# Kernel tuning notes

Measured on AMD Instinct MI355X. Metric: run time of the kernel, lower is better.

## Reference

```python
import jax, jax.numpy as jnp
import numpy as np

B, NUM_CLASSES, G = 8, 80, 100
IMG = 1280
STRIDES = (8, 16, 32)
EPS = 1e-7            # mmyolo EPS in -log(iou + EPS)
IOU_EPS = 1e-6        # BboxOverlaps2D union eps
INF = 1e8
SOFT_CENTER_RADIUS = 3.0
TOPK = 13
IOU_WEIGHT = 3.0


def _make_priors():
    ps = []
    for s in STRIDES:
        n = IMG // s
        c = (jnp.arange(n, dtype=jnp.float32) + 0.5) * s
        yy, xx = jnp.meshgrid(c, c, indexing='ij')
        st = jnp.full((n * n,), float(s), jnp.float32)
        ps.append(jnp.stack([xx.ravel(), yy.ravel(), st, st], axis=-1))
    return jnp.concatenate(ps, axis=0)  # [N, 4] = (cx, cy, stride_x, stride_y)


def setup_inputs() -> dict:
    key = jax.random.key(0)
    k = jax.random.split(key, 8)
    priors = _make_priors()
    N = priors.shape[0]  # 33600
    # predicted boxes jittered around anchor points, xyxy
    cxcy = priors[None, :, :2] + jax.random.normal(k[0], (B, N, 2)) * priors[None, :, 2:3] * 2.0
    wh = priors[None, :, 2:3] * (1.0 + 4.0 * jax.random.uniform(k[1], (B, N, 2)))
    pred_bboxes = jnp.concatenate([cxcy - wh / 2, cxcy + wh / 2], axis=-1)
    pred_scores = jax.random.normal(k[2], (B, N, NUM_CLASSES)) * 2.0 - 2.0  # logits
    # gt boxes inside the image, xyxy
    x1y1 = jax.random.uniform(k[3], (B, G, 2)) * (IMG - 200)
    gwh = 20.0 + jax.random.uniform(k[4], (B, G, 2)) * 180.0
    gt_bboxes = jnp.concatenate([x1y1, x1y1 + gwh], axis=-1)
    gt_labels = jax.random.randint(k[5], (B, G, 1), 0, NUM_CLASSES)
    counts = jax.random.randint(k[6], (B,), 10, G + 1)
    pad_bbox_flag = (jnp.arange(G)[None, :] < counts[:, None]).astype(jnp.float32)[..., None]
    return {"pred_bboxes": pred_bboxes, "pred_scores": pred_scores, "priors": priors,
            "gt_labels": gt_labels, "gt_bboxes": gt_bboxes, "pad_bbox_flag": pad_bbox_flag}


def _pairwise_iou(b1, b2):
    # b1 [B,N,4], b2 [B,G,4] in xyxy -> [B,N,G]
    a1 = (b1[..., 2] - b1[..., 0]) * (b1[..., 3] - b1[..., 1])
    a2 = (b2[..., 2] - b2[..., 0]) * (b2[..., 3] - b2[..., 1])
    lt = jnp.maximum(b1[:, :, None, :2], b2[:, None, :, :2])
    rb = jnp.minimum(b1[:, :, None, 2:], b2[:, None, :, 2:])
    wh = jnp.clip(rb - lt, 0.0)
    overlap = wh[..., 0] * wh[..., 1]
    union = a1[:, :, None] + a2[:, None, :] - overlap
    return overlap / jnp.maximum(union, IOU_EPS)


def reference(pred_bboxes, pred_scores, priors, gt_labels, gt_bboxes, pad_bbox_flag):
    Bb, N, _ = pred_bboxes.shape
    Gg = gt_bboxes.shape[1]
    centers = priors[:, :2]
    valid_gt = pad_bbox_flag[..., 0] > 0  # [B,G]

    # point-in-box test (strict >0, as in find_inside_points)
    lt = centers[None, :, None, :] - gt_bboxes[:, None, :, :2]   # [B,N,G,2]
    rb = gt_bboxes[:, None, :, 2:] - centers[None, :, None, :]
    is_in = (jnp.minimum(jnp.min(lt, -1), jnp.min(rb, -1)) > 0) & valid_gt[:, None, :]
    valid_mask = jnp.any(is_in, -1)  # [B,N]

    # soft center prior
    gt_center = (gt_bboxes[..., :2] + gt_bboxes[..., 2:]) / 2.0
    strides = priors[:, 2]
    dist = jnp.sqrt(jnp.sum((centers[None, :, None, :] - gt_center[:, None, :, :]) ** 2, -1))
    dist = dist / strides[None, :, None] * valid_mask[..., None].astype(dist.dtype)
    soft_center_prior = jnp.power(10.0, dist - SOFT_CENTER_RADIUS)

    # IoU cost
    ious = _pairwise_iou(pred_bboxes, gt_bboxes)  # [B,N,G]
    iou_cost = -jnp.log(ious + EPS) * IOU_WEIGHT

    # classification cost: gather pred score of each gt's class
    lbl = jnp.broadcast_to(gt_labels[:, None, :, 0], (Bb, N, Gg))
    x = jnp.take_along_axis(pred_scores, lbl, axis=2)  # logits [B,N,G]
    scale = ious - jax.nn.sigmoid(x)
    bce = jax.nn.softplus(x) - x * ious  # BCE-with-logits, target=ious
    cls_cost = bce * (scale * scale)

    cost = cls_cost + iou_cost + soft_center_prior
    cost = jnp.where(valid_mask[..., None], cost, INF)

    # dynamic k per gt = clamp(int(sum of top-13 ious), min 1)
    k = min(TOPK, N)
    topk_ious = jax.lax.top_k(jnp.swapaxes(ious, 1, 2), k)[0]  # [B,G,k]
    dyn_k = jnp.maximum(jnp.sum(topk_ious, -1).astype(jnp.int32), 1)  # [B,G]

    # rank of each prior's cost within its gt column (ascending)
    ranks = jnp.argsort(jnp.argsort(cost, axis=1), axis=1)
    matching = (ranks < dyn_k[:, None, :]) & valid_gt[:, None, :]  # [B,N,G]

    # resolve priors matched to multiple gts: keep min-cost gt
    multi = jnp.sum(matching, -1) > 1  # [B,N]
    argmin_g = jnp.argmin(cost, axis=-1)
    onehot = argmin_g[..., None] == jnp.arange(Gg)[None, None, :]
    matching = jnp.where(multi[..., None], onehot, matching)

    fg = jnp.any(matching, -1)                       # [B,N]
    matched_gt = jnp.argmax(matching, -1)            # [B,N]
    matched_ious = jnp.sum(jnp.where(matching, ious, 0.0), -1)

    lbls = jnp.take_along_axis(gt_labels[..., 0], matched_gt, axis=1)
    assigned_labels = jnp.where(fg, lbls, NUM_CLASSES)
    assigned_labels_weights = jnp.ones((Bb, N), pred_scores.dtype)
    boxes = jnp.take_along_axis(gt_bboxes, matched_gt[..., None], axis=1)
    assigned_bboxes = jnp.where(fg[..., None], boxes, 0.0)
    assign_metrics = jnp.where(fg, matched_ious, 0.0)
    return assigned_labels, assigned_labels_weights, assigned_bboxes, assign_metrics
```

## Files before the change

kernel.cpp:

```cpp
#include <hip/hip_runtime.h>
#include <stdint.h>

#define BDIM 256
#define B_   8
#define NCLS 80
#define G_   100
#define N_   33600
#define TOPK_ 13
#define NCHUNK 2
#define TILES 525
#define CAPC 160
#define CAPI 160
#define INFC 1e8f


__device__ __forceinline__ unsigned int fkey(float f){
  unsigned int u = __float_as_uint(f);
  return (u & 0x80000000u) ? ~u : (u | 0x80000000u);
}
__device__ __forceinline__ float unfkey(unsigned int k){
  unsigned int u = (k & 0x80000000u) ? (k & 0x7fffffffu) : ~k;
  return __uint_as_float(u);
}

__device__ __forceinline__ float cost_eval(float iou, float x, float dist, bool valid){
  #pragma clang fp contract(off)
  float prior = exp2f((dist - 3.0f) * 3.321928094887362f);
  float iouc  = -logf(iou + 1e-7f) * 3.0f;
  float sig   = 1.0f / (1.0f + expf(-x));
  float sc    = iou - sig;
  float bce   = fmaxf(x, 0.0f) + log1pf(expf(-fabsf(x))) - x * iou;
  float c     = bce * (sc * sc) + iouc + prior;
  return valid ? c : INFC;
}

__device__ __forceinline__ unsigned long long wave_min_u64(unsigned long long v){
  #pragma unroll
  for (int m = 1; m < 64; m <<= 1){
    unsigned int lo = (unsigned int)__shfl_xor((int)(unsigned int)v, m, 64);
    unsigned int hi = (unsigned int)__shfl_xor((int)(unsigned int)(v >> 32), m, 64);
    unsigned long long o = ((unsigned long long)hi << 32) | lo;
    v = o < v ? o : v;
  }
  return v;
}

__device__ __forceinline__ void tile_params(int t, int& W, int& base, int& trow, int& tcol,
                                            float& s, float& invs){
  if (t < 400){            W = 160; base = 0;     s = 8.0f;  invs = 0.125f;
    trow = (t/20)*8;  tcol = (t - (t/20)*20)*8; }
  else if (t < 500){ int u = t - 400; W = 80; base = 25600; s = 16.0f; invs = 0.0625f;
    trow = (u/10)*8; tcol = (u - (u/10)*10)*8; }
  else {             int u = t - 500; W = 40; base = 32000; s = 32.0f; invs = 0.03125f;
    trow = (u/5)*8;  tcol = (u - (u/5)*5)*8; }
}

__device__ unsigned long long compact_cost(unsigned long long* buf, int cnt){
  const int lane = threadIdx.x & 63;
  unsigned long long a0 = (lane       < cnt) ? buf[lane]       : ~0ull;
  unsigned long long a1 = (lane + 64  < cnt) ? buf[lane + 64]  : ~0ull;
  unsigned long long a2 = (lane + 128 < cnt) ? buf[lane + 128] : ~0ull;
  unsigned long long mykeep = ~0ull, t13 = ~0ull;
  #pragma unroll
  for (int r = 0; r < TOPK_; ++r){
    unsigned long long v = a0 < a1 ? a0 : a1; v = v < a2 ? v : a2;
    unsigned long long mn = wave_min_u64(v);
    if      (a0 == mn) a0 = ~0ull;
    else if (a1 == mn) a1 = ~0ull;
    else if (a2 == mn) a2 = ~0ull;
    if (lane == r) mykeep = mn;
    t13 = mn;
  }
  if (lane < TOPK_) buf[lane] = mykeep;
  return t13;
}

__device__ float compact_iou(float* buf, int cnt){
  const int lane = threadIdx.x & 63;
  float a0 = (lane       < cnt) ? buf[lane]       : -1.0f;
  float a1 = (lane + 64  < cnt) ? buf[lane + 64]  : -1.0f;
  float a2 = (lane + 128 < cnt) ? buf[lane + 128] : -1.0f;
  float mykeep = -1.0f, t13 = -1.0f;
  #pragma unroll
  for (int r = 0; r < TOPK_; ++r){
    float mx = fmaxf(fmaxf(a0, a1), a2);
    #pragma unroll
    for (int m = 1; m < 64; m <<= 1) mx = fmaxf(mx, __shfl_xor(mx, m, 64));
    bool h0 = (a0 == mx), h1 = (a1 == mx), h2 = (a2 == mx);
    unsigned long long ball = __ballot(h0 | h1 | h2);
    int src = (int)(__ffsll(ball) - 1);
    if (lane == src){
      if (h0) a0 = -1.0f; else if (h1) a1 = -1.0f; else a2 = -1.0f;
    }
    if (lane == r) mykeep = mx;
    t13 = mx;
  }
  if (lane < TOPK_) buf[lane] = mykeep;
  return t13;
}


__global__ void __launch_bounds__(BDIM) k_validmask(
    const float* __restrict__ priors,
    const float* __restrict__ gt_bboxes,
    const float* __restrict__ pad_flag,
    unsigned char* __restrict__ valid_mask,
    uint32_t* __restrict__ match_mask)
{
  int b = blockIdx.y;
  __shared__ float4 sbox[G_];
  __shared__ float  sflag[G_];
  for (int g = threadIdx.x; g < G_; g += BDIM){
    sbox[g]  = ((const float4*)gt_bboxes)[b*G_ + g];
    sflag[g] = pad_flag[b*G_ + g];
  }
  __syncthreads();
  int n = blockIdx.x*BDIM + threadIdx.x;
  if (n >= N_) return;
  float cx = priors[n*4+0], cy = priors[n*4+1];
  bool v = false;
  for (int g = 0; g < G_; ++g){
    float4 gb = sbox[g];
    bool in = (cx - gb.x > 0.0f) & (cy - gb.y > 0.0f) &
              (gb.z - cx > 0.0f) & (gb.w - cy > 0.0f) & (sflag[g] > 0.0f);
    v |= in;
  }
  size_t idx = (size_t)b*N_ + n;
  valid_mask[idx] = v ? 1 : 0;
  ((uint4*)match_mask)[idx] = make_uint4(0u,0u,0u,0u);
}


__global__ void __launch_bounds__(64) k_tileprep(
    const float* __restrict__ pred_bboxes,
    const unsigned char* __restrict__ valid_mask,
    float4* __restrict__ tile_agg,
    uint32_t* __restrict__ tile_flag)
{
  int t = blockIdx.x, b = blockIdx.y, l = threadIdx.x;
  int W, base, trow, tcol; float s, invs;
  tile_params(t, W, base, trow, tcol, s, invs);
  int n = base + (trow + (l >> 3))*W + tcol + (l & 7);
  size_t idx = (size_t)b*N_ + n;
  float4 pb = ((const float4*)pred_bboxes)[idx];
  int v = valid_mask[idx];
  float x1 = pb.x, y1 = pb.y, x2 = pb.z, y2 = pb.w;
  #pragma unroll
  for (int m = 1; m < 64; m <<= 1){
    x1 = fminf(x1, __shfl_xor(x1, m, 64));
    y1 = fminf(y1, __shfl_xor(y1, m, 64));
    x2 = fmaxf(x2, __shfl_xor(x2, m, 64));
    y2 = fmaxf(y2, __shfl_xor(y2, m, 64));
  }
  unsigned long long anyb = __ballot(v != 0);
  if (l == 0){
    tile_agg [(size_t)b*TILES + t] = make_float4(x1, y1, x2, y2);
    tile_flag[(size_t)b*TILES + t] = (anyb != 0ull) ? 1u : 0u;
  }
}


__global__ void __launch_bounds__(BDIM) k_topk(
    const float* __restrict__ pred_bboxes,
    const float* __restrict__ pred_scores,
    const int*   __restrict__ gt_labels,
    const float* __restrict__ gt_bboxes,
    const float* __restrict__ pad_flag,
    const unsigned char* __restrict__ valid_mask,
    const float4* __restrict__ tile_agg,
    const uint32_t* __restrict__ tile_flag,
    unsigned long long* __restrict__ ck_out,
    float* __restrict__ ci_out)
{
  #pragma clang fp contract(off)
  const int g = blockIdx.x, b = blockIdx.y, chunk = blockIdx.z;
  if (pad_flag[b*G_ + g] <= 0.0f) return;

  __shared__ unsigned long long s_cbuf[4][CAPC];
  __shared__ float s_ibuf[4][CAPI];
  __shared__ unsigned long long s_fk[4][TOPK_ + 1];
  __shared__ float s_fi[4][TOPK_ + 1];

  const int tid = threadIdx.x, lane = tid & 63, wid = tid >> 6;
  unsigned long long* cbuf = s_cbuf[wid];
  float* ibuf = s_ibuf[wid];

  const float4 gb = ((const float4*)gt_bboxes)[b*G_ + g];
  const float ga  = (gb.z - gb.x) * (gb.w - gb.y);
  const float gcx = (gb.x + gb.z) * 0.5f, gcy = (gb.y + gb.w) * 0.5f;
  const int lbl = gt_labels[b*G_ + g];
  const unsigned int KEYINF = fkey(INFC);

  const float4* pb4 = (const float4*)pred_bboxes + (size_t)b*N_;
  const unsigned char* vm = valid_mask + (size_t)b*N_;
  const float* sc_b = pred_scores + (size_t)b*N_*NCLS;
  const float4* tag = tile_agg + (size_t)b*TILES;
  const uint32_t* tfl = tile_flag + (size_t)b*TILES;

  auto seed_eval = [&](int t, float& cst, float& iouv){
    #pragma clang fp contract(off)
    int nk, bs; float s, invs;
    if      (t < 25){ nk = 160; bs = 0;     s = 8.0f;  invs = 0.125f;   }
    else if (t < 50){ nk = 80;  bs = 25600; s = 16.0f; invs = 0.0625f;  }
    else            { nk = 40;  bs = 32000; s = 32.0f; invs = 0.03125f; }
    int rem = (t < 25) ? t : ((t < 50) ? t - 25 : t - 50);
    int r = rem / 5, c = rem - 5*r;
    int ix = (int)(gcx / s) - 2, iy = (int)(gcy / s) - 2;
    ix = ix < 0 ? 0 : (ix > nk-5 ? nk-5 : ix);
    iy = iy < 0 ? 0 : (iy > nk-5 ? nk-5 : iy);
    int col = ix + c, row = iy + r;
    int n = bs + row*nk + col;
    float4 pb = pb4[n];
    float pa = (pb.z - pb.x) * (pb.w - pb.y);
    float lx = fmaxf(pb.x, gb.x), ly = fmaxf(pb.y, gb.y);
    float rx = fminf(pb.z, gb.z), ry = fminf(pb.w, gb.w);
    float ov = fmaxf(rx - lx, 0.0f) * fmaxf(ry - ly, 0.0f);
    float un = pa + ga - ov;
    float iou = ov / fmaxf(un, 1e-6f);
    iouv = iou;
    bool valid = vm[n] != 0;
    float px = ((float)col + 0.5f)*s, py = ((float)row + 0.5f)*s;
    float dx = px - gcx, dy = py - gcy;
    float dist = sqrtf(dx*dx + dy*dy) * invs;
    float x = valid ? sc_b[(size_t)n*NCLS + lbl] : 0.0f;
    cst = cost_eval(iou, x, dist, valid);
  };

  float c0 = 3e38f, c1 = 3e38f, i0 = -1.0f, i1 = -1.0f;
  seed_eval(lane, c0, i0);
  if (lane < 11) seed_eval(lane + 64, c1, i1);

  float T = INFC;
  {
    const float lvs[7] = {47.0f, 24.0f, 12.0f, 6.0f, 3.0f, 1.5f, 0.75f};
    #pragma unroll
    for (int i = 0; i < 7; ++i){
      int cnt = __popcll(__ballot(c0 <= lvs[i])) + __popcll(__ballot(c1 <= lvs[i]));
      if (cnt >= TOPK_) T = lvs[i];
    }
  }
  float Tiou_m = 0.0f;
  {
    const float ivs[8] = {0.02f, 0.05f, 0.1f, 0.15f, 0.22f, 0.3f, 0.4f, 0.5f};
    #pragma unroll
    for (int i = 0; i < 8; ++i){
      int cnt = __popcll(__ballot(i0 >= ivs[i])) + __popcll(__ballot(i1 >= ivs[i]));
      if (cnt >= TOPK_) Tiou_m = ivs[i] * 0.999f;
    }
  }
  unsigned long long Tkey = ((unsigned long long)fkey(T) << 32) | 0xFFFFFFFFull;
  bool  tc48  = T < 48.0f;
  float gt_   = 3.02f + log10f(T);
  float gthr2 = gt_ * gt_;

  int ccnt = 0, icnt = 0;

  int sweep_nend = 0;
  if (chunk == 0 && wid == 0 && T == INFC){
    int found = 0, base = 0;
    while (found < TOPK_ && base < N_){
      int n = base + lane;
      bool inv = (vm[n] == 0);
      unsigned long long m = __ballot(inv);
      int pc = __popcll(m);
      int pos = ccnt + (int)__popcll(m & ((1ull << lane) - 1ull));
      if (inv) cbuf[pos] = ((unsigned long long)KEYINF << 32) | (unsigned)n;
      ccnt += pc;
      found += pc;
      base += 64;
    }
    sweep_nend = base;
  }

  const int lo_c = (chunk == 0) ? 0 : 263;
  const int hi_c = (chunk == 0) ? 263 : TILES;
  const int per  = (hi_c - lo_c + 3) >> 2;
  const int lo_w = lo_c + wid*per;
  const int hi_w = min(hi_c, lo_w + per);

  for (int tb = lo_w; tb < hi_w; tb += 64){
    int tt2 = tb + lane;
    bool pass = false;
    if (tt2 < hi_w){
      float4 ag = tag[tt2];
      uint32_t fl2 = tfl[tt2];
      int W, bse, trow, tcol; float s, invs;
      tile_params(tt2, W, bse, trow, tcol, s, invs);
      bool inter = (fminf(ag.z, gb.z) > fmaxf(ag.x, gb.x)) &&
                   (fminf(ag.w, gb.w) > fmaxf(ag.y, gb.y));
      float rx0 = ((float)tcol + 0.5f)*s, rx1 = ((float)tcol + 7.5f)*s;
      float ry0 = ((float)trow + 0.5f)*s, ry1 = ((float)trow + 7.5f)*s;
      float ddx = fmaxf(0.0f, fmaxf(rx0 - gcx, gcx - rx1));
      float ddy = fmaxf(0.0f, fmaxf(ry0 - gcy, gcy - ry1));
      float md2s = (ddx*ddx + ddy*ddy) * (invs*invs);
      bool costok = (fl2 != 0) && (md2s <= gthr2) && (inter || !tc48);
      pass = inter || costok;
    }
    unsigned long long pm = __ballot(pass);
    while (pm){
      int bit = (int)(__ffsll(pm) - 1);
      pm &= pm - 1ull;
      const int tt = tb + bit;

      int W, bse, trow, tcol; float s, invs;
      tile_params(tt, W, bse, trow, tcol, s, invs);
      int row = trow + (lane >> 3), col = tcol + (lane & 7);
      int n = bse + row*W + col;
      float px = ((float)col + 0.5f)*s, py = ((float)row + 0.5f)*s;
      float4 pb = pb4[n];
      float pa = (pb.z - pb.x) * (pb.w - pb.y);
      float lx = fmaxf(pb.x, gb.x), ly = fmaxf(pb.y, gb.y);
      float rx = fminf(pb.z, gb.z), ry = fminf(pb.w, gb.w);
      float ov = fmaxf(rx - lx, 0.0f) * fmaxf(ry - ly, 0.0f);
      float un = pa + ga - ov;
      bool ipass = ov > Tiou_m * un;

      float dx = px - gcx, dy = py - gcy;
      float dist2 = dx*dx + dy*dy;
      float d2s = dist2 * (invs * invs);
      bool valid = vm[n] != 0;
      bool needcost = valid && (d2s <= gthr2) && !((ov <= 0.0f) && tc48);

      float iou = 0.0f;
      if (__any(ipass || needcost)){
        if (ipass || needcost) iou = ov / fmaxf(un, 1e-6f);
      }

      {
        unsigned long long m = __ballot(ipass);
        if (m){
          int pc = __popcll(m);
          if (icnt + pc > CAPI){
            float t = compact_iou(ibuf, icnt); icnt = TOPK_;
            Tiou_m = t * 0.999f;
          }
          int pos = icnt + (int)__popcll(m & ((1ull << lane) - 1ull));
          if (ipass) ibuf[pos] = iou;
          icnt += pc;
        }
      }

      unsigned long long key = ((unsigned long long)KEYINF << 32) | (unsigned)n;
      bool cpass = (!valid) && (key < Tkey) && (n >= sweep_nend);
      if (__any(needcost)){
        if (needcost){
          float x = sc_b[(size_t)n*NCLS + lbl];
          float dist = sqrtf(dist2) * invs;
          float c = cost_eval(iou, x, dist, true);
          key = ((unsigned long long)fkey(c) << 32) | (unsigned)n;
          cpass = key < Tkey;
        }
      }
      {
        unsigned long long m = __ballot(cpass);
        if (m){
          int pc = __popcll(m);
          if (ccnt + pc > CAPC){
            Tkey = compact_cost(cbuf, ccnt); ccnt = TOPK_;
            float Tc = unfkey((unsigned int)(Tkey >> 32));
            tc48 = Tc < 48.0f;
            float gq = 3.02f + log10f(Tc);
            gthr2 = (gq > 0.0f) ? gq*gq : 1e30f;
          }
          int pos = ccnt + (int)__popcll(m & ((1ull << lane) - 1ull));
          if (cpass) cbuf[pos] = key;
          ccnt += pc;
        }
      }
    }
  }

  compact_cost(cbuf, ccnt);
  compact_iou(ibuf, icnt);
  if (lane < TOPK_){ s_fk[wid][lane] = cbuf[lane]; s_fi[wid][lane] = ibuf[lane]; }
  if (lane == TOPK_){ s_fk[wid][TOPK_] = ~0ull; s_fi[wid][TOPK_] = -1e30f; }
  __syncthreads();

  if (tid == 0){
    size_t base = (((size_t)b*G_ + g)*NCHUNK + chunk)*TOPK_;
    {
      int p0 = 0, p1 = 0, p2 = 0, p3 = 0;
      for (int r = 0; r < TOPK_; ++r){
        float v0 = s_fi[0][p0], v1 = s_fi[1][p1], v2 = s_fi[2][p2], v3 = s_fi[3][p3];
        float mx = fmaxf(fmaxf(v0, v1), fmaxf(v2, v3));
        if      (v0 == mx) p0++;
        else if (v1 == mx) p1++;
        else if (v2 == mx) p2++;
        else               p3++;
        ci_out[base + r] = mx;
      }
    }
    {
      int q0 = 0, q1 = 0, q2 = 0, q3 = 0;
      for (int r = 0; r < TOPK_; ++r){
        unsigned long long k0 = s_fk[0][q0], k1 = s_fk[1][q1];
        unsigned long long k2 = s_fk[2][q2], k3 = s_fk[3][q3];
        unsigned long long mn = k0 < k1 ? k0 : k1;
        unsigned long long mn2 = k2 < k3 ? k2 : k3;
        mn = mn < mn2 ? mn : mn2;
        if      (k0 == mn) q0++;
        else if (k1 == mn) q1++;
        else if (k2 == mn) q2++;
        else               q3++;
        ck_out[base + r] = mn;
      }
    }
  }
}


__global__ void __launch_bounds__(64) k_merge(
    const float* __restrict__ pad_flag,
    const unsigned long long* __restrict__ ck,
    const float* __restrict__ ci,
    uint32_t* __restrict__ match_mask)
{
  const int g = blockIdx.x, b = blockIdx.y;
  if (threadIdx.x != 0) return;
  if (pad_flag[b*G_ + g] <= 0.0f) return;

  const size_t base = ((size_t)b*G_ + g)*NCHUNK*TOPK_;
  const unsigned long long* K = ck + base;
  const float* I = ci + base;

  int p0 = 0, p1 = 0; float s = 0.0f;
  for (int r = 0; r < TOPK_; ++r){
    float v0 = (p0 < TOPK_) ? I[p0]          : -1e30f;
    float v1 = (p1 < TOPK_) ? I[TOPK_ + p1]  : -1e30f;
    float mx = fmaxf(v0, v1);
    if (v0 == mx) p0++; else p1++;
    s += fmaxf(mx, 0.0f);
  }
  int dynk = (int)s;
  if (dynk < 1) dynk = 1;
  if (dynk > TOPK_) dynk = TOPK_;

  int q0 = 0, q1 = 0;
  for (int r = 0; r < dynk; ++r){
    unsigned long long k0 = (q0 < TOPK_) ? K[q0]         : ~0ull;
    unsigned long long k1 = (q1 < TOPK_) ? K[TOPK_ + q1] : ~0ull;
    unsigned long long mn = k0 < k1 ? k0 : k1;
    if (k0 == mn) q0++; else q1++;
    int n = (int)(mn & 0xffffffffu);
    if (n < N_)
      atomicOr(&match_mask[((size_t)b*N_ + n)*4 + (g >> 5)], 1u << (g & 31));
  }
}


__global__ void __launch_bounds__(BDIM) k_assign(
    const float* __restrict__ pred_bboxes,
    const float* __restrict__ pred_scores,
    const float* __restrict__ priors,
    const int*   __restrict__ gt_labels,
    const float* __restrict__ gt_bboxes,
    const unsigned char* __restrict__ valid_mask,
    const uint32_t* __restrict__ match_mask,
    float* __restrict__ out)
{
  #pragma clang fp contract(off)
  const int b = blockIdx.y;
  __shared__ float4 sbox[G_];
  __shared__ int    slbl[G_];
  __shared__ float  sga[G_], sgcx[G_], sgcy[G_];
  for (int g = threadIdx.x; g < G_; g += BDIM){
    float4 q = ((const float4*)gt_bboxes)[b*G_ + g];
    sbox[g] = q; slbl[g] = gt_labels[b*G_ + g];
    sga[g]  = (q.z - q.x) * (q.w - q.y);
    sgcx[g] = (q.x + q.z) * 0.5f;
    sgcy[g] = (q.y + q.w) * 0.5f;
  }
  __syncthreads();
  int n = blockIdx.x*BDIM + threadIdx.x;
  if (n >= N_) return;
  const int lane = threadIdx.x & 63;
  size_t idx = (size_t)b*N_ + n;
  uint4 mm = ((const uint4*)match_mask)[idx];
  int count = __popc(mm.x) + __popc(mm.y) + __popc(mm.z) + __popc(mm.w);

  float lblv = (float)NCLS;
  float4 ob = make_float4(0.f, 0.f, 0.f, 0.f);
  float met = 0.0f;

  if (__any(count > 0)){
    float4 pb = make_float4(0.f,0.f,0.f,0.f); float pa = 0.0f;
    if (count > 0){
      pb = ((const float4*)pred_bboxes)[idx];
      pa = (pb.z - pb.x) * (pb.w - pb.y);
    }
    if (count == 1){
      int mg = mm.x ? (__ffs(mm.x) - 1) :
               mm.y ? (31 + __ffs(mm.y)) :
               mm.z ? (63 + __ffs(mm.z)) : (95 + __ffs(mm.w));
      float4 q = sbox[mg];
      float lx = fmaxf(pb.x, q.x), ly = fmaxf(pb.y, q.y);
      float rx = fminf(pb.z, q.z), ry = fminf(pb.w, q.w);
      float ov = fmaxf(rx - lx, 0.0f) * fmaxf(ry - ly, 0.0f);
      float iou = ov / fmaxf(pa + sga[mg] - ov, 1e-6f);
      lblv = (float)slbl[mg]; ob = q; met = iou;
    }
    unsigned long long heavy = __ballot(count > 1);
    if (heavy){
      float4 pr = make_float4(0.f,0.f,0.f,0.f); int hv0 = 0;
      if (count > 1){
        pr = ((const float4*)priors)[n];
        hv0 = valid_mask[idx];
      }
      while (heavy){
        int src = (int)(__ffsll(heavy) - 1);
        heavy &= heavy - 1ull;
        float hx1 = __shfl(pb.x, src, 64), hy1 = __shfl(pb.y, src, 64);
        float hx2 = __shfl(pb.z, src, 64), hy2 = __shfl(pb.w, src, 64);
        float hpa = __shfl(pa,   src, 64);
        float hcx = __shfl(pr.x, src, 64), hcy = __shfl(pr.y, src, 64);
        float hst = __shfl(pr.z, src, 64);
        int   hv  = __shfl(hv0,  src, 64);
        int   hn  = __shfl(n,    src, 64);
        float hinvs = __uint_as_float(0x7F000000u - __float_as_uint(hst));
        const float* hrow = pred_scores + ((size_t)b*N_ + hn)*(size_t)NCLS;

        unsigned long long bk = ~0ull;
        #pragma unroll
        for (int h = 0; h < 2; ++h){
          int g = lane + h*64;
          if (g < G_){
            float4 q = sbox[g];
            float lx = fmaxf(hx1, q.x), ly = fmaxf(hy1, q.y);
            float rx = fminf(hx2, q.z), ry = fminf(hy2, q.w);
            float ov = fmaxf(rx - lx, 0.0f) * fmaxf(ry - ly, 0.0f);
            float un = hpa + sga[g] - ov;
            float iou = ov / fmaxf(un, 1e-6f);
            float dx = hcx - sgcx[g], dy = hcy - sgcy[g];
            float dist = sqrtf(dx*dx + dy*dy) * hinvs;
            float x = hrow[slbl[g]];
            float c = cost_eval(iou, x, dist, hv != 0);
            unsigned long long key = ((unsigned long long)fkey(c) << 32) | (unsigned)g;
            bk = key < bk ? key : bk;
          }
        }
        bk = wave_min_u64(bk);
        if (lane == src){
          int gw = (int)(bk & 0xffffffffu);
          float4 q = sbox[gw];
          float lx = fmaxf(pb.x, q.x), ly = fmaxf(pb.y, q.y);
          float rx = fminf(pb.z, q.z), ry = fminf(pb.w, q.w);
          float ov = fmaxf(rx - lx, 0.0f) * fmaxf(ry - ly, 0.0f);
          met  = ov / fmaxf(pa + sga[gw] - ov, 1e-6f);
          lblv = (float)slbl[gw];
          ob = q;
        }
      }
    }
  }

  out[idx] = lblv;
  out[(size_t)B_*N_ + idx] = 1.0f;
  ((float4*)(out + (size_t)2*B_*N_))[idx] = ob;
  out[(size_t)6*B_*N_ + idx] = met;
}


extern "C" void kernel_launch(void* const* d_in, const int* in_sizes, int n_in,
                              void* d_out, int out_size, void* d_ws, size_t ws_size,
                              hipStream_t stream) {
  const float* pred_bboxes = (const float*)d_in[0];
  const float* pred_scores = (const float*)d_in[1];
  const float* priors      = (const float*)d_in[2];
  const int*   gt_labels   = (const int*)  d_in[3];
  const float* gt_bboxes   = (const float*)d_in[4];
  const float* pad_flag    = (const float*)d_in[5];
  float* out = (float*)d_out;

  const size_t MASK_B  = (size_t)B_*N_*4*sizeof(uint32_t);
  const size_t VALID_B = ((size_t)B_*N_ + 255) & ~(size_t)255;
  const size_t CK_B    = (size_t)B_*G_*NCHUNK*TOPK_*sizeof(unsigned long long);
  const size_t CI_B    = (size_t)B_*G_*NCHUNK*TOPK_*sizeof(float);
  const size_t AGG_B   = (size_t)B_*TILES*sizeof(float4);
  uint32_t* match_mask = (uint32_t*)d_ws;
  unsigned char* valid_mask = (unsigned char*)d_ws + MASK_B;
  unsigned long long* ck = (unsigned long long*)((char*)d_ws + MASK_B + VALID_B);
  float* ci = (float*)((char*)d_ws + MASK_B + VALID_B + CK_B);
  float4* tile_agg = (float4*)((char*)d_ws + MASK_B + VALID_B + CK_B + CI_B);
  uint32_t* tile_flag = (uint32_t*)((char*)d_ws + MASK_B + VALID_B + CK_B + CI_B + AGG_B);

  dim3 gridN((N_ + BDIM - 1)/BDIM, B_);
  dim3 gridT(TILES, B_);
  dim3 gridG(G_, B_, NCHUNK);
  dim3 gridM(G_, B_);

  k_validmask<<<gridN, BDIM, 0, stream>>>(priors, gt_bboxes, pad_flag,
                                          valid_mask, match_mask);
  k_tileprep<<<gridT, 64, 0, stream>>>(pred_bboxes, valid_mask, tile_agg, tile_flag);
  k_topk<<<gridG, BDIM, 0, stream>>>(pred_bboxes, pred_scores, gt_labels,
                                     gt_bboxes, pad_flag, valid_mask,
                                     tile_agg, tile_flag, ck, ci);
  k_merge<<<gridM, 64, 0, stream>>>(pad_flag, ck, ci, match_mask);
  k_assign<<<gridN, BDIM, 0, stream>>>(pred_bboxes, pred_scores, priors, gt_labels,
                                       gt_bboxes, valid_mask, match_mask, out);
}
```

Measured before the change: 76.67 us.

## Fuse prep kernels and merge top-k chunks into single 8-wave block per gt

Merges the valid-mask and tile-prep kernels into one tile-indexed kernel that derives prior centres from the tile coordinates instead of reading them from memory. The top-k kernel now uses one 512-thread block per gt instead of two 256-thread chunk blocks, merges the per-wave top-13 lists in shared memory and writes the match mask directly. This removes the separate merge kernel and the global ck/ci scratch round trip, cutting two launches. In exchange there are half as many top-k blocks, each with more waves, plus an extra barrier after the seed thresholds are computed by wave 0.

```diff
diff --git a/kernel.cpp b/kernel.cpp
--- a/kernel.cpp
+++ b/kernel.cpp
@@ -2,13 +2,14 @@
 #include <stdint.h>
 
 #define BDIM 256
+#define TDIM 512
 #define B_   8
 #define NCLS 80
 #define G_   100
 #define N_   33600
 #define TOPK_ 13
-#define NCHUNK 2
 #define TILES 525
+#define NW   8
 #define CAPC 160
 #define CAPI 160
 #define INFC 1e8f
@@ -100,24 +101,30 @@
 }
 
 
-__global__ void __launch_bounds__(BDIM) k_validmask(
-    const float* __restrict__ priors,
+__global__ void __launch_bounds__(64) k_prep(
+    const float* __restrict__ pred_bboxes,
     const float* __restrict__ gt_bboxes,
     const float* __restrict__ pad_flag,
     unsigned char* __restrict__ valid_mask,
-    uint32_t* __restrict__ match_mask)
+    uint32_t* __restrict__ match_mask,
+    float4* __restrict__ tile_agg,
+    uint32_t* __restrict__ tile_flag)
 {
-  int b = blockIdx.y;
+  const int t = blockIdx.x, b = blockIdx.y, l = threadIdx.x;
   __shared__ float4 sbox[G_];
   __shared__ float  sflag[G_];
-  for (int g = threadIdx.x; g < G_; g += BDIM){
+  for (int g = l; g < G_; g += 64){
     sbox[g]  = ((const float4*)gt_bboxes)[b*G_ + g];
     sflag[g] = pad_flag[b*G_ + g];
   }
   __syncthreads();
-  int n = blockIdx.x*BDIM + threadIdx.x;
-  if (n >= N_) return;
-  float cx = priors[n*4+0], cy = priors[n*4+1];
+
+  int W, base, trow, tcol; float s, invs;
+  tile_params(t, W, base, trow, tcol, s, invs);
+  int row = trow + (l >> 3), col = tcol + (l & 7);
+  int n = base + row*W + col;
+  float cx = ((float)col + 0.5f)*s, cy = ((float)row + 0.5f)*s;
+
   bool v = false;
   for (int g = 0; g < G_; ++g){
     float4 gb = sbox[g];
@@ -128,22 +135,8 @@
   size_t idx = (size_t)b*N_ + n;
   valid_mask[idx] = v ? 1 : 0;
   ((uint4*)match_mask)[idx] = make_uint4(0u,0u,0u,0u);
-}
-
-
-__global__ void __launch_bounds__(64) k_tileprep(
-    const float* __restrict__ pred_bboxes,
-    const unsigned char* __restrict__ valid_mask,
-    float4* __restrict__ tile_agg,
-    uint32_t* __restrict__ tile_flag)
-{
-  int t = blockIdx.x, b = blockIdx.y, l = threadIdx.x;
-  int W, base, trow, tcol; float s, invs;
-  tile_params(t, W, base, trow, tcol, s, invs);
-  int n = base + (trow + (l >> 3))*W + tcol + (l & 7);
-  size_t idx = (size_t)b*N_ + n;
+
   float4 pb = ((const float4*)pred_bboxes)[idx];
-  int v = valid_mask[idx];
   float x1 = pb.x, y1 = pb.y, x2 = pb.z, y2 = pb.w;
   #pragma unroll
   for (int m = 1; m < 64; m <<= 1){
@@ -152,7 +145,7 @@
     x2 = fmaxf(x2, __shfl_xor(x2, m, 64));
     y2 = fmaxf(y2, __shfl_xor(y2, m, 64));
   }
-  unsigned long long anyb = __ballot(v != 0);
+  unsigned long long anyb = __ballot(v);
   if (l == 0){
     tile_agg [(size_t)b*TILES + t] = make_float4(x1, y1, x2, y2);
     tile_flag[(size_t)b*TILES + t] = (anyb != 0ull) ? 1u : 0u;
@@ -160,7 +153,7 @@
 }
 
 
-__global__ void __launch_bounds__(BDIM) k_topk(
+__global__ void __launch_bounds__(TDIM) k_topk(
     const float* __restrict__ pred_bboxes,
     const float* __restrict__ pred_scores,
     const int*   __restrict__ gt_labels,
@@ -169,17 +162,17 @@
     const unsigned char* __restrict__ valid_mask,
     const float4* __restrict__ tile_agg,
     const uint32_t* __restrict__ tile_flag,
-    unsigned long long* __restrict__ ck_out,
-    float* __restrict__ ci_out)
+    uint32_t* __restrict__ match_mask)
 {
   #pragma clang fp contract(off)
-  const int g = blockIdx.x, b = blockIdx.y, chunk = blockIdx.z;
+  const int g = blockIdx.x, b = blockIdx.y;
   if (pad_flag[b*G_ + g] <= 0.0f) return;
 
-  __shared__ unsigned long long s_cbuf[4][CAPC];
-  __shared__ float s_ibuf[4][CAPI];
-  __shared__ unsigned long long s_fk[4][TOPK_ + 1];
-  __shared__ float s_fi[4][TOPK_ + 1];
+  __shared__ unsigned long long s_cbuf[NW][CAPC];
+  __shared__ float s_ibuf[NW][CAPI];
+  __shared__ unsigned long long s_fk[NW*TOPK_];
+  __shared__ float s_fi[NW*TOPK_];
+  __shared__ float s_thr[2];
 
   const int tid = threadIdx.x, lane = tid & 63, wid = tid >> 6;
   unsigned long long* cbuf = s_cbuf[wid];
@@ -197,86 +190,91 @@
   const float4* tag = tile_agg + (size_t)b*TILES;
   const uint32_t* tfl = tile_flag + (size_t)b*TILES;
 
-  auto seed_eval = [&](int t, float& cst, float& iouv){
-    #pragma clang fp contract(off)
-    int nk, bs; float s, invs;
-    if      (t < 25){ nk = 160; bs = 0;     s = 8.0f;  invs = 0.125f;   }
-    else if (t < 50){ nk = 80;  bs = 25600; s = 16.0f; invs = 0.0625f;  }
-    else            { nk = 40;  bs = 32000; s = 32.0f; invs = 0.03125f; }
-    int rem = (t < 25) ? t : ((t < 50) ? t - 25 : t - 50);
-    int r = rem / 5, c = rem - 5*r;
-    int ix = (int)(gcx / s) - 2, iy = (int)(gcy / s) - 2;
-    ix = ix < 0 ? 0 : (ix > nk-5 ? nk-5 : ix);
-    iy = iy < 0 ? 0 : (iy > nk-5 ? nk-5 : iy);
-    int col = ix + c, row = iy + r;
-    int n = bs + row*nk + col;
-    float4 pb = pb4[n];
-    float pa = (pb.z - pb.x) * (pb.w - pb.y);
-    float lx = fmaxf(pb.x, gb.x), ly = fmaxf(pb.y, gb.y);
-    float rx = fminf(pb.z, gb.z), ry = fminf(pb.w, gb.w);
-    float ov = fmaxf(rx - lx, 0.0f) * fmaxf(ry - ly, 0.0f);
-    float un = pa + ga - ov;
-    float iou = ov / fmaxf(un, 1e-6f);
-    iouv = iou;
-    bool valid = vm[n] != 0;
-    float px = ((float)col + 0.5f)*s, py = ((float)row + 0.5f)*s;
-    float dx = px - gcx, dy = py - gcy;
-    float dist = sqrtf(dx*dx + dy*dy) * invs;
-    float x = valid ? sc_b[(size_t)n*NCLS + lbl] : 0.0f;
-    cst = cost_eval(iou, x, dist, valid);
-  };
-
-  float c0 = 3e38f, c1 = 3e38f, i0 = -1.0f, i1 = -1.0f;
-  seed_eval(lane, c0, i0);
-  if (lane < 11) seed_eval(lane + 64, c1, i1);
-
-  float T = INFC;
-  {
-    const float lvs[7] = {47.0f, 24.0f, 12.0f, 6.0f, 3.0f, 1.5f, 0.75f};
-    #pragma unroll
-    for (int i = 0; i < 7; ++i){
-      int cnt = __popcll(__ballot(c0 <= lvs[i])) + __popcll(__ballot(c1 <= lvs[i]));
-      if (cnt >= TOPK_) T = lvs[i];
-    }
-  }
-  float Tiou_m = 0.0f;
-  {
-    const float ivs[8] = {0.02f, 0.05f, 0.1f, 0.15f, 0.22f, 0.3f, 0.4f, 0.5f};
-    #pragma unroll
-    for (int i = 0; i < 8; ++i){
-      int cnt = __popcll(__ballot(i0 >= ivs[i])) + __popcll(__ballot(i1 >= ivs[i]));
-      if (cnt >= TOPK_) Tiou_m = ivs[i] * 0.999f;
-    }
-  }
-  unsigned long long Tkey = ((unsigned long long)fkey(T) << 32) | 0xFFFFFFFFull;
-  bool  tc48  = T < 48.0f;
-  float gt_   = 3.02f + log10f(T);
+  if (wid == 0){
+    auto seed_eval = [&](int t, float& cst, float& iouv){
+      #pragma clang fp contract(off)
+      int nk, bs; float s, invs;
+      if      (t < 25){ nk = 160; bs = 0;     s = 8.0f;  invs = 0.125f;   }
+      else if (t < 50){ nk = 80;  bs = 25600; s = 16.0f; invs = 0.0625f;  }
+      else            { nk = 40;  bs = 32000; s = 32.0f; invs = 0.03125f; }
+      int rem = (t < 25) ? t : ((t < 50) ? t - 25 : t - 50);
+      int r = rem / 5, c = rem - 5*r;
+      int ix = (int)(gcx / s) - 2, iy = (int)(gcy / s) - 2;
+      ix = ix < 0 ? 0 : (ix > nk-5 ? nk-5 : ix);
+      iy = iy < 0 ? 0 : (iy > nk-5 ? nk-5 : iy);
+      int col = ix + c, row = iy + r;
+      int n = bs + row*nk + col;
+      float4 pb = pb4[n];
+      float pa = (pb.z - pb.x) * (pb.w - pb.y);
+      float lx = fmaxf(pb.x, gb.x), ly = fmaxf(pb.y, gb.y);
+      float rx = fminf(pb.z, gb.z), ry = fminf(pb.w, gb.w);
+      float ov = fmaxf(rx - lx, 0.0f) * fmaxf(ry - ly, 0.0f);
+      float un = pa + ga - ov;
+      float iou = ov / fmaxf(un, 1e-6f);
+      iouv = iou;
+      bool valid = vm[n] != 0;
+      float px = ((float)col + 0.5f)*s, py = ((float)row + 0.5f)*s;
+      float dx = px - gcx, dy = py - gcy;
+      float dist = sqrtf(dx*dx + dy*dy) * invs;
+      float x = valid ? sc_b[(size_t)n*NCLS + lbl] : 0.0f;
+      cst = cost_eval(iou, x, dist, valid);
+    };
+    float c0 = 3e38f, c1 = 3e38f, i0 = -1.0f, i1 = -1.0f;
+    seed_eval(lane, c0, i0);
+    if (lane < 11) seed_eval(lane + 64, c1, i1);
+    float T = INFC;
+    {
+      const float lvs[7] = {47.0f, 24.0f, 12.0f, 6.0f, 3.0f, 1.5f, 0.75f};
+      #pragma unroll
+      for (int i = 0; i < 7; ++i){
+        int cnt = __popcll(__ballot(c0 <= lvs[i])) + __popcll(__ballot(c1 <= lvs[i]));
+        if (cnt >= TOPK_) T = lvs[i];
+      }
+    }
+    float Ti = 0.0f;
+    {
+      const float ivs[8] = {0.02f, 0.05f, 0.1f, 0.15f, 0.22f, 0.3f, 0.4f, 0.5f};
+      #pragma unroll
+      for (int i = 0; i < 8; ++i){
+        int cnt = __popcll(__ballot(i0 >= ivs[i])) + __popcll(__ballot(i1 >= ivs[i]));
+        if (cnt >= TOPK_) Ti = ivs[i] * 0.999f;
+      }
+    }
+    if (lane == 0){ s_thr[0] = T; s_thr[1] = Ti; }
+  }
+  __syncthreads();
+
+  const float T0 = s_thr[0];
+  float Tiou_m = s_thr[1];
+  unsigned long long Tkey = ((unsigned long long)fkey(T0) << 32) | 0xFFFFFFFFull;
+  bool  tc48  = T0 < 48.0f;
+  float gt_   = 3.02f + log10f(T0);
   float gthr2 = gt_ * gt_;
 
   int ccnt = 0, icnt = 0;
 
   int sweep_nend = 0;
-  if (chunk == 0 && wid == 0 && T == INFC){
+  if (T0 == INFC){
     int found = 0, base = 0;
     while (found < TOPK_ && base < N_){
       int n = base + lane;
       bool inv = (vm[n] == 0);
       unsigned long long m = __ballot(inv);
       int pc = __popcll(m);
-      int pos = ccnt + (int)__popcll(m & ((1ull << lane) - 1ull));
-      if (inv) cbuf[pos] = ((unsigned long long)KEYINF << 32) | (unsigned)n;
-      ccnt += pc;
+      if (wid == 0){
+        int pos = ccnt + (int)__popcll(m & ((1ull << lane) - 1ull));
+        if (inv) cbuf[pos] = ((unsigned long long)KEYINF << 32) | (unsigned)n;
+        ccnt += pc;
+      }
       found += pc;
       base += 64;
     }
     sweep_nend = base;
   }
 
-  const int lo_c = (chunk == 0) ? 0 : 263;
-  const int hi_c = (chunk == 0) ? 263 : TILES;
-  const int per  = (hi_c - lo_c + 3) >> 2;
-  const int lo_w = lo_c + wid*per;
-  const int hi_w = min(hi_c, lo_w + per);
+  const int per  = (TILES + NW - 1) / NW;
+  const int lo_w = wid*per;
+  const int hi_w = min(TILES, lo_w + per);
 
   for (int tb = lo_w; tb < hi_w; tb += 64){
     int tt2 = tb + lane;
@@ -372,78 +370,26 @@
 
   compact_cost(cbuf, ccnt);
   compact_iou(ibuf, icnt);
-  if (lane < TOPK_){ s_fk[wid][lane] = cbuf[lane]; s_fi[wid][lane] = ibuf[lane]; }
-  if (lane == TOPK_){ s_fk[wid][TOPK_] = ~0ull; s_fi[wid][TOPK_] = -1e30f; }
+  if (lane < TOPK_){ s_fk[wid*TOPK_ + lane] = cbuf[lane]; s_fi[wid*TOPK_ + lane] = ibuf[lane]; }
   __syncthreads();
 
+  if (wid == 0){
+    compact_cost(s_fk, NW*TOPK_);
+    compact_iou(s_fi, NW*TOPK_);
+  }
+  __syncthreads();
+
   if (tid == 0){
-    size_t base = (((size_t)b*G_ + g)*NCHUNK + chunk)*TOPK_;
-    {
-      int p0 = 0, p1 = 0, p2 = 0, p3 = 0;
-      for (int r = 0; r < TOPK_; ++r){
-        float v0 = s_fi[0][p0], v1 = s_fi[1][p1], v2 = s_fi[2][p2], v3 = s_fi[3][p3];
-        float mx = fmaxf(fmaxf(v0, v1), fmaxf(v2, v3));
-        if      (v0 == mx) p0++;
-        else if (v1 == mx) p1++;
-        else if (v2 == mx) p2++;
-        else               p3++;
-        ci_out[base + r] = mx;
-      }
-    }
-    {
-      int q0 = 0, q1 = 0, q2 = 0, q3 = 0;
-      for (int r = 0; r < TOPK_; ++r){
-        unsigned long long k0 = s_fk[0][q0], k1 = s_fk[1][q1];
-        unsigned long long k2 = s_fk[2][q2], k3 = s_fk[3][q3];
-        unsigned long long mn = k0 < k1 ? k0 : k1;
-        unsigned long long mn2 = k2 < k3 ? k2 : k3;
-        mn = mn < mn2 ? mn : mn2;
-        if      (k0 == mn) q0++;
-        else if (k1 == mn) q1++;
-        else if (k2 == mn) q2++;
-        else               q3++;
-        ck_out[base + r] = mn;
-      }
-    }
-  }
-}
-
-
-__global__ void __launch_bounds__(64) k_merge(
-    const float* __restrict__ pad_flag,
-    const unsigned long long* __restrict__ ck,
-    const float* __restrict__ ci,
-    uint32_t* __restrict__ match_mask)
-{
-  const int g = blockIdx.x, b = blockIdx.y;
-  if (threadIdx.x != 0) return;
-  if (pad_flag[b*G_ + g] <= 0.0f) return;
-
-  const size_t base = ((size_t)b*G_ + g)*NCHUNK*TOPK_;
-  const unsigned long long* K = ck + base;
-  const float* I = ci + base;
-
-  int p0 = 0, p1 = 0; float s = 0.0f;
-  for (int r = 0; r < TOPK_; ++r){
-    float v0 = (p0 < TOPK_) ? I[p0]          : -1e30f;
-    float v1 = (p1 < TOPK_) ? I[TOPK_ + p1]  : -1e30f;
-    float mx = fmaxf(v0, v1);
-    if (v0 == mx) p0++; else p1++;
-    s += fmaxf(mx, 0.0f);
-  }
-  int dynk = (int)s;
-  if (dynk < 1) dynk = 1;
-  if (dynk > TOPK_) dynk = TOPK_;
-
-  int q0 = 0, q1 = 0;
-  for (int r = 0; r < dynk; ++r){
-    unsigned long long k0 = (q0 < TOPK_) ? K[q0]         : ~0ull;
-    unsigned long long k1 = (q1 < TOPK_) ? K[TOPK_ + q1] : ~0ull;
-    unsigned long long mn = k0 < k1 ? k0 : k1;
-    if (k0 == mn) q0++; else q1++;
-    int n = (int)(mn & 0xffffffffu);
-    if (n < N_)
-      atomicOr(&match_mask[((size_t)b*N_ + n)*4 + (g >> 5)], 1u << (g & 31));
+    float ssum = 0.0f;
+    for (int r = 0; r < TOPK_; ++r) ssum += fmaxf(s_fi[r], 0.0f);
+    int dynk = (int)ssum;
+    if (dynk < 1) dynk = 1;
+    if (dynk > TOPK_) dynk = TOPK_;
+    for (int r = 0; r < dynk; ++r){
+      int n = (int)(s_fk[r] & 0xffffffffu);
+      if (n < N_)
+        atomicOr(&match_mask[((size_t)b*N_ + n)*4 + (g >> 5)], 1u << (g & 31));
+    }
   }
 }
 
@@ -573,28 +519,21 @@
 
   const size_t MASK_B  = (size_t)B_*N_*4*sizeof(uint32_t);
   const size_t VALID_B = ((size_t)B_*N_ + 255) & ~(size_t)255;
-  const size_t CK_B    = (size_t)B_*G_*NCHUNK*TOPK_*sizeof(unsigned long long);
-  const size_t CI_B    = (size_t)B_*G_*NCHUNK*TOPK_*sizeof(float);
   const size_t AGG_B   = (size_t)B_*TILES*sizeof(float4);
   uint32_t* match_mask = (uint32_t*)d_ws;
   unsigned char* valid_mask = (unsigned char*)d_ws + MASK_B;
-  unsigned long long* ck = (unsigned long long*)((char*)d_ws + MASK_B + VALID_B);
-  float* ci = (float*)((char*)d_ws + MASK_B + VALID_B + CK_B);
-  float4* tile_agg = (float4*)((char*)d_ws + MASK_B + VALID_B + CK_B + CI_B);
-  uint32_t* tile_flag = (uint32_t*)((char*)d_ws + MASK_B + VALID_B + CK_B + CI_B + AGG_B);
-
+  float4* tile_agg = (float4*)((char*)d_ws + MASK_B + VALID_B);
+  uint32_t* tile_flag = (uint32_t*)((char*)d_ws + MASK_B + VALID_B + AGG_B);
+
+  dim3 gridT(TILES, B_);
+  dim3 gridG(G_, B_);
   dim3 gridN((N_ + BDIM - 1)/BDIM, B_);
-  dim3 gridT(TILES, B_);
-  dim3 gridG(G_, B_, NCHUNK);
-  dim3 gridM(G_, B_);
-
-  k_validmask<<<gridN, BDIM, 0, stream>>>(priors, gt_bboxes, pad_flag,
-                                          valid_mask, match_mask);
-  k_tileprep<<<gridT, 64, 0, stream>>>(pred_bboxes, valid_mask, tile_agg, tile_flag);
-  k_topk<<<gridG, BDIM, 0, stream>>>(pred_bboxes, pred_scores, gt_labels,
+
+  k_prep<<<gridT, 64, 0, stream>>>(pred_bboxes, gt_bboxes, pad_flag,
+                                   valid_mask, match_mask, tile_agg, tile_flag);
+  k_topk<<<gridG, TDIM, 0, stream>>>(pred_bboxes, pred_scores, gt_labels,
                                      gt_bboxes, pad_flag, valid_mask,
-                                     tile_agg, tile_flag, ck, ci);
-  k_merge<<<gridM, 64, 0, stream>>>(pad_flag, ck, ci, match_mask);
+                                     tile_agg, tile_flag, match_mask);
   k_assign<<<gridN, BDIM, 0, stream>>>(pred_bboxes, pred_scores, priors, gt_labels,
                                        gt_bboxes, valid_mask, match_mask, out);
 }
```

New measurement: 72.86 us. -5.0%, faster.
